# Kernel tuning notes

Measured on AMD Instinct MI355X. Metric: run time of the kernel, lower is better.

The kernel has to match this reference:

```python
import jax, jax.numpy as jnp
import numpy as np

B, C, H, W = 16, 8, 512, 512
EPS_TH = 1e-14

def setup_inputs() -> dict:
    key = jax.random.key(0)
    x = jax.random.normal(key, (B, C, H, W), dtype=jnp.float32)
    alpha = jnp.full((1,), 0.95, dtype=jnp.float32)
    beta = jnp.full((1,), 8.0, dtype=jnp.float32)
    return {"x": x, "alpha": alpha, "beta": beta}

def reference(x, alpha, beta):
    b, c, h, w = x.shape
    x2 = x.reshape(b * c, h * w)
    # torch.nanquantile with default linear interpolation == jnp.nanquantile
    i1 = jnp.nanquantile(x2, 0.01, axis=1, keepdims=True)   # [B*C, 1]
    i99 = jnp.nanquantile(x2, 0.99, axis=1, keepdims=True)  # [B*C, 1]
    th = (i1 + (i99 - i1) * alpha).reshape(b, c, 1, 1)      # broadcast instead of tile
    mask = (th > EPS_TH).astype(x.dtype)
    th_new = th * mask + (1.0 - mask)
    gate = 1.0 / (1.0 + jnp.exp(-(beta / th_new * (jnp.abs(x) - th * mask))))
    return jax.nn.relu(x) * gate
```

## Files before the change

kernel.cpp:

```cpp
#include <hip/hip_runtime.h>


#define ROWS 128
#define NPR  262144
#define BINS 8192
#define SHIFT 19
#define CAP  4096
#define QTPB 1024
#define OTPB 256

#define K_LO 2621u
#define K_HI 259521u

__device__ __forceinline__ unsigned keyOf(float f) {
    unsigned u = __float_as_uint(f);
    return (u & 0x80000000u) ? ~u : (u | 0x80000000u);
}
__device__ __forceinline__ float keyToFloat(unsigned k) {
    unsigned u = (k & 0x80000000u) ? (k & 0x7fffffffu) : ~k;
    return __uint_as_float(u);
}

__global__ __launch_bounds__(QTPB) void k_quant(const float* __restrict__ x,
                                                float* __restrict__ qv) {
    const int row = blockIdx.x;
    const int tid = threadIdx.x;
    const float4* xr = (const float4*)(x + (size_t)row * NPR);

    __shared__ unsigned smem[BINS];
    unsigned* hist = smem;
    unsigned (*cand)[CAP] = (unsigned(*)[CAP])smem;
    __shared__ unsigned part[256];
    __shared__ unsigned sh[256];
    __shared__ unsigned sb[8];
    __shared__ unsigned svar[4];
    __shared__ unsigned ccnt[2];

    for (int i = tid; i < BINS; i += QTPB) hist[i] = 0;
    __syncthreads();

    const int NV = NPR / 4;
    for (int i = tid; i < NV; i += QTPB) {
        float4 v = xr[i];
        atomicAdd(&hist[keyOf(v.x) >> SHIFT], 1u);
        atomicAdd(&hist[keyOf(v.y) >> SHIFT], 1u);
        atomicAdd(&hist[keyOf(v.z) >> SHIFT], 1u);
        atomicAdd(&hist[keyOf(v.w) >> SHIFT], 1u);
    }
    __syncthreads();

    const int CH = BINS / 256;
    if (tid < 256) {
        unsigned s = 0;
        int base = tid * CH;
        for (int i = 0; i < CH; ++i) s += hist[base + i];
        part[tid] = s;
    }
    __syncthreads();
    if (tid == 0) {
        unsigned run = 0;
        for (int t = 0; t < 256; ++t) { unsigned tmp = part[t]; part[t] = run; run += tmp; }
    }
    __syncthreads();
    if (tid < 256) {
        unsigned cum = part[tid];
        int base = tid * CH;
        const unsigned targets[4] = {K_LO, K_LO + 1u, K_HI, K_HI + 1u};
        for (int i = 0; i < CH; ++i) {
            unsigned c = hist[base + i];
            if (c) {
                #pragma unroll
                for (int t = 0; t < 4; ++t) {
                    if (targets[t] >= cum && targets[t] < cum + c) {
                        if      (t == 0) { sb[0] = base + i; sb[2] = cum; }
                        else if (t == 1) { sb[1] = base + i; }
                        else if (t == 2) { sb[3] = base + i; sb[5] = cum; }
                        else             { sb[4] = base + i; }
                    }
                }
            }
            cum += c;
        }
    }
    if (tid < 2) ccnt[tid] = 0;
    __syncthreads();

    {
        unsigned blo0 = sb[0], bhi0 = sb[1], blo1 = sb[3], bhi1 = sb[4];
        for (int i = tid; i < NV; i += QTPB) {
            float4 v = xr[i];
            float vv[4] = {v.x, v.y, v.z, v.w};
            #pragma unroll
            for (int j = 0; j < 4; ++j) {
                unsigned key = keyOf(vv[j]);
                unsigned bin = key >> SHIFT;
                if (bin >= blo0 && bin <= bhi0) {
                    unsigned p = atomicAdd(&ccnt[0], 1u);
                    if (p < CAP) cand[0][p] = key;
                }
                if (bin >= blo1 && bin <= bhi1) {
                    unsigned p = atomicAdd(&ccnt[1], 1u);
                    if (p < CAP) cand[1][p] = key;
                }
            }
        }
    }
    __syncthreads();

    for (int iq = 0; iq < 2; ++iq) {
        unsigned m = ccnt[iq]; if (m > CAP) m = CAP;
        unsigned cb = iq ? sb[5] : sb[2];
        unsigned t_lo = (iq ? K_HI : K_LO) - cb;
        unsigned prefix = 0, trem = t_lo, cntEq = 0;
        for (int p = 3; p >= 0; --p) {
            for (int i = tid; i < 256; i += QTPB) sh[i] = 0;
            __syncthreads();
            for (unsigned i = tid; i < m; i += QTPB) {
                unsigned key = cand[iq][i];
                bool match = (p == 3) || ((key >> ((p + 1) * 8)) == (prefix >> ((p + 1) * 8)));
                if (match) atomicAdd(&sh[(key >> (p * 8)) & 255u], 1u);
            }
            __syncthreads();
            if (tid == 0) {
                unsigned cum = 0;
                for (int b = 0; b < 256; ++b) {
                    unsigned c = sh[b];
                    if (trem >= cum && trem < cum + c) { svar[0] = (unsigned)b; svar[1] = cum; svar[2] = c; break; }
                    cum += c;
                }
            }
            __syncthreads();
            prefix |= svar[0] << (p * 8);
            trem   -= svar[1];
            cntEq   = svar[2];
            __syncthreads();
        }
        unsigned vlo_key = prefix;
        unsigned cntLess = t_lo - trem;
        unsigned vhi_key;
        if (t_lo + 1u < cntLess + cntEq) {
            vhi_key = vlo_key;
        } else {
            if (tid == 0) svar[3] = 0xFFFFFFFFu;
            __syncthreads();
            for (unsigned i = tid; i < m; i += QTPB) {
                unsigned key = cand[iq][i];
                if (key > vlo_key) atomicMin(&svar[3], key);
            }
            __syncthreads();
            vhi_key = svar[3];
        }
        if (tid == 0) {
            double frac = iq ? (0.99 * (double)(NPR - 1) - (double)K_HI)
                             : (0.01 * (double)(NPR - 1) - (double)K_LO);
            double vlo = (double)keyToFloat(vlo_key);
            double vhi = (double)keyToFloat(vhi_key);
            qv[row * 2 + iq] = (float)(vlo + (vhi - vlo) * frac);
        }
        __syncthreads();
    }
}

__global__ __launch_bounds__(OTPB) void k_out(const float* __restrict__ x,
                                              const float* __restrict__ alpha,
                                              const float* __restrict__ beta,
                                              const float* __restrict__ qv,
                                              float* __restrict__ out) {
    float a  = alpha[0];
    float bt = beta[0];
    const int nvec = ROWS * (NPR / 4);
    int stride = gridDim.x * blockDim.x;
    for (int i = blockIdx.x * blockDim.x + threadIdx.x; i < nvec; i += stride) {
        int row = i >> 16;
        float q0 = qv[row * 2], q1 = qv[row * 2 + 1];
        float th = q0 + (q1 - q0) * a;
        bool  msk = th > 1e-14f;
        float thn = msk ? th : 1.0f;
        float scale = bt / thn;
        float thm = msk ? th : 0.0f;
        float4 v = ((const float4*)x)[i];
        float4 o;
        o.x = v.x > 0.f ? v.x / (1.f + __expf(-(scale * (fabsf(v.x) - thm)))) : 0.f;
        o.y = v.y > 0.f ? v.y / (1.f + __expf(-(scale * (fabsf(v.y) - thm)))) : 0.f;
        o.z = v.z > 0.f ? v.z / (1.f + __expf(-(scale * (fabsf(v.z) - thm)))) : 0.f;
        o.w = v.w > 0.f ? v.w / (1.f + __expf(-(scale * (fabsf(v.w) - thm)))) : 0.f;
        ((float4*)out)[i] = o;
    }
}

extern "C" void kernel_launch(void* const* d_in, const int* in_sizes, int n_in,
                              void* d_out, int out_size, void* d_ws, size_t ws_size,
                              hipStream_t stream) {
    const float* x     = (const float*)d_in[0];
    const float* alpha = (const float*)d_in[1];
    const float* beta  = (const float*)d_in[2];
    float* out = (float*)d_out;
    float* qv  = (float*)d_ws;
    k_quant<<<ROWS, QTPB, 0, stream>>>(x, qv);
    k_out  <<<2048, OTPB, 0, stream>>>(x, alpha, beta, qv, out);
}
```

Baseline: 419.4 us.

## Split histogram pass across multiple blocks per row and streamline output kernel

Moves the first histogram pass out of the single-block-per-row quantile kernel into a separate kernel that uses eight blocks per row. Each block builds a shared-memory partial histogram and merges it into a global per-row histogram with atomics. The selection kernel then loads that histogram instead of rebuilding it. The output kernel now computes per-row threshold parameters once per block and uses native exp2/rcp intrinsics. This adds a memset, an extra launch and global atomic merges, but raises parallelism for the histogram pass, which was limited to 128 blocks.

```diff
diff --git a/kernel.cpp b/kernel.cpp
--- a/kernel.cpp
+++ b/kernel.cpp
@@ -6,6 +6,8 @@
 #define BINS 8192
 #define SHIFT 19
 #define CAP  4096
+#define HTPB 256
+#define HBPR 8
 #define QTPB 1024
 #define OTPB 256
 
@@ -21,14 +23,38 @@
     return __uint_as_float(u);
 }
 
-__global__ __launch_bounds__(QTPB) void k_quant(const float* __restrict__ x,
-                                                float* __restrict__ qv) {
+__global__ __launch_bounds__(HTPB) void k_hist(const float* __restrict__ x,
+                                               unsigned* __restrict__ gh) {
+    __shared__ unsigned lh[BINS];
+    for (int i = threadIdx.x; i < BINS; i += HTPB) lh[i] = 0;
+    __syncthreads();
+    const int row = blockIdx.x >> 3;
+    const int blk = blockIdx.x & 7;
+    const float4* xr = (const float4*)(x + (size_t)row * NPR + (size_t)blk * (NPR / HBPR));
+    const int NV = NPR / HBPR / 4;
+    for (int i = threadIdx.x; i < NV; i += HTPB) {
+        float4 v = xr[i];
+        atomicAdd(&lh[keyOf(v.x) >> SHIFT], 1u);
+        atomicAdd(&lh[keyOf(v.y) >> SHIFT], 1u);
+        atomicAdd(&lh[keyOf(v.z) >> SHIFT], 1u);
+        atomicAdd(&lh[keyOf(v.w) >> SHIFT], 1u);
+    }
+    __syncthreads();
+    unsigned* h = gh + (size_t)row * BINS;
+    for (int i = threadIdx.x; i < BINS; i += HTPB) {
+        unsigned c = lh[i];
+        if (c) atomicAdd(&h[i], c);
+    }
+}
+
+__global__ __launch_bounds__(QTPB) void k_qsel(const float* __restrict__ x,
+                                               const unsigned* __restrict__ gh,
+                                               float* __restrict__ qv) {
     const int row = blockIdx.x;
     const int tid = threadIdx.x;
     const float4* xr = (const float4*)(x + (size_t)row * NPR);
 
     __shared__ unsigned smem[BINS];
-    unsigned* hist = smem;
     unsigned (*cand)[CAP] = (unsigned(*)[CAP])smem;
     __shared__ unsigned part[256];
     __shared__ unsigned sh[256];
@@ -36,24 +62,15 @@
     __shared__ unsigned svar[4];
     __shared__ unsigned ccnt[2];
 
-    for (int i = tid; i < BINS; i += QTPB) hist[i] = 0;
-    __syncthreads();
-
-    const int NV = NPR / 4;
-    for (int i = tid; i < NV; i += QTPB) {
-        float4 v = xr[i];
-        atomicAdd(&hist[keyOf(v.x) >> SHIFT], 1u);
-        atomicAdd(&hist[keyOf(v.y) >> SHIFT], 1u);
-        atomicAdd(&hist[keyOf(v.z) >> SHIFT], 1u);
-        atomicAdd(&hist[keyOf(v.w) >> SHIFT], 1u);
-    }
+    const unsigned* h = gh + (size_t)row * BINS;
+    for (int i = tid; i < BINS; i += QTPB) smem[i] = h[i];
     __syncthreads();
 
     const int CH = BINS / 256;
     if (tid < 256) {
         unsigned s = 0;
         int base = tid * CH;
-        for (int i = 0; i < CH; ++i) s += hist[base + i];
+        for (int i = 0; i < CH; ++i) s += smem[base + i];
         part[tid] = s;
     }
     __syncthreads();
@@ -67,7 +84,7 @@
         int base = tid * CH;
         const unsigned targets[4] = {K_LO, K_LO + 1u, K_HI, K_HI + 1u};
         for (int i = 0; i < CH; ++i) {
-            unsigned c = hist[base + i];
+            unsigned c = smem[base + i];
             if (c) {
                 #pragma unroll
                 for (int t = 0; t < 4; ++t) {
@@ -87,6 +104,7 @@
 
     {
         unsigned blo0 = sb[0], bhi0 = sb[1], blo1 = sb[3], bhi1 = sb[4];
+        const int NV = NPR / 4;
         for (int i = tid; i < NV; i += QTPB) {
             float4 v = xr[i];
             float vv[4] = {v.x, v.y, v.z, v.w};
@@ -166,25 +184,26 @@
                                               const float* __restrict__ beta,
                                               const float* __restrict__ qv,
                                               float* __restrict__ out) {
-    float a  = alpha[0];
-    float bt = beta[0];
-    const int nvec = ROWS * (NPR / 4);
-    int stride = gridDim.x * blockDim.x;
-    for (int i = blockIdx.x * blockDim.x + threadIdx.x; i < nvec; i += stride) {
-        int row = i >> 16;
-        float q0 = qv[row * 2], q1 = qv[row * 2 + 1];
-        float th = q0 + (q1 - q0) * a;
-        bool  msk = th > 1e-14f;
-        float thn = msk ? th : 1.0f;
-        float scale = bt / thn;
-        float thm = msk ? th : 0.0f;
-        float4 v = ((const float4*)x)[i];
+    const int row = blockIdx.x >> 4;
+    float q0 = qv[row * 2], q1 = qv[row * 2 + 1];
+    float a = alpha[0], bt = beta[0];
+    float th = q0 + (q1 - q0) * a;
+    bool  msk = th > 1e-14f;
+    float thn = msk ? th : 1.0f;
+    float thm = msk ? th : 0.0f;
+    float nsc = -(bt / thn) * 1.4426950408889634f;
+    const float4* xv = (const float4*)x + (size_t)blockIdx.x * 4096;
+    float4*       ov = (float4*)out     + (size_t)blockIdx.x * 4096;
+    #pragma unroll 4
+    for (int k = 0; k < 16; ++k) {
+        int i = k * OTPB + threadIdx.x;
+        float4 v = xv[i];
         float4 o;
-        o.x = v.x > 0.f ? v.x / (1.f + __expf(-(scale * (fabsf(v.x) - thm)))) : 0.f;
-        o.y = v.y > 0.f ? v.y / (1.f + __expf(-(scale * (fabsf(v.y) - thm)))) : 0.f;
-        o.z = v.z > 0.f ? v.z / (1.f + __expf(-(scale * (fabsf(v.z) - thm)))) : 0.f;
-        o.w = v.w > 0.f ? v.w / (1.f + __expf(-(scale * (fabsf(v.w) - thm)))) : 0.f;
-        ((float4*)out)[i] = o;
+        o.x = v.x > 0.f ? v.x * __builtin_amdgcn_rcpf(1.f + __builtin_amdgcn_exp2f(nsc * (fabsf(v.x) - thm))) : 0.f;
+        o.y = v.y > 0.f ? v.y * __builtin_amdgcn_rcpf(1.f + __builtin_amdgcn_exp2f(nsc * (fabsf(v.y) - thm))) : 0.f;
+        o.z = v.z > 0.f ? v.z * __builtin_amdgcn_rcpf(1.f + __builtin_amdgcn_exp2f(nsc * (fabsf(v.z) - thm))) : 0.f;
+        o.w = v.w > 0.f ? v.w * __builtin_amdgcn_rcpf(1.f + __builtin_amdgcn_exp2f(nsc * (fabsf(v.w) - thm))) : 0.f;
+        ov[i] = o;
     }
 }
 
@@ -195,7 +214,10 @@
     const float* alpha = (const float*)d_in[1];
     const float* beta  = (const float*)d_in[2];
     float* out = (float*)d_out;
-    float* qv  = (float*)d_ws;
-    k_quant<<<ROWS, QTPB, 0, stream>>>(x, qv);
-    k_out  <<<2048, OTPB, 0, stream>>>(x, alpha, beta, qv, out);
-}
+    unsigned* gh = (unsigned*)d_ws;
+    float* qv = (float*)(gh + (size_t)ROWS * BINS);
+    hipMemsetAsync(gh, 0, (size_t)ROWS * BINS * sizeof(unsigned), stream);
+    k_hist<<<ROWS * HBPR, HTPB, 0, stream>>>(x, gh);
+    k_qsel<<<ROWS,        QTPB, 0, stream>>>(x, gh, qv);
+    k_out <<<ROWS * 16,   OTPB, 0, stream>>>(x, alpha, beta, qv, out);
+}
```

Measured after the change: 419.8 us. Within noise of the previous version (+0.1%).
